# Kernel optimization log

Hardware: AMD Instinct MI355X
Metric: run time of the kernel (lower is better)

Reference implementation:

```python
import math
import jax, jax.numpy as jnp
import numpy as np

HEADS = 8
DIM_HEAD = 64
NUM_MEM_KV = 16


def alibi_slopes(heads):
    def pow2_slopes(n):
        start = 2 ** (-(2 ** -(math.log2(n) - 3)))
        return [start * (start ** i) for i in range(n)]
    if math.log2(heads).is_integer():
        return np.asarray(pow2_slopes(heads), dtype=np.float32)
    cp2 = 2 ** math.floor(math.log2(heads))
    extra = pow2_slopes(2 * cp2)[0::2][: heads - cp2]
    return np.asarray(pow2_slopes(cp2) + extra, dtype=np.float32)


def setup_inputs() -> dict:
    key = jax.random.key(0)
    ks = jax.random.split(key, 12)
    b, n, dim = 2, 2048, 512
    h, dh, mem = HEADS, DIM_HEAD, NUM_MEM_KV
    s = 0.02  # weight init scale for numerical sanity
    return {
        "x": jax.random.normal(ks[0], (b, n, dim), jnp.float32),
        "Wq": jax.random.normal(ks[1], (dim, h * dh), jnp.float32) * s,
        "Wk": jax.random.normal(ks[2], (dim, h * dh), jnp.float32) * s,
        "Wv": jax.random.normal(ks[3], (dim, h * dh), jnp.float32) * s,
        "mem_k": jax.random.normal(ks[4], (h, mem, dh), jnp.float32),
        "mem_v": jax.random.normal(ks[5], (h, mem, dh), jnp.float32),
        "pre_proj": jax.random.normal(ks[6], (h, h), jnp.float32),
        "post_proj": jax.random.normal(ks[7], (h, h), jnp.float32),
        "head_scale_params": jnp.ones((1, h, 1, 1), jnp.float32),
        "Wout": jax.random.normal(ks[8], (h * dh, dim), jnp.float32) * s,
        "bout": jnp.zeros((dim,), jnp.float32),
    }


def reference(x, Wq, Wk, Wv, mem_k, mem_v, pre_proj, post_proj,
              head_scale_params, Wout, bout):
    b, n, dim = x.shape
    h, dh, mem = HEADS, DIM_HEAD, NUM_MEM_KV
    scale = dh ** -0.5

    def split_heads(t):  # [b,n,h*dh] -> [b,h,n,dh]
        return t.reshape(b, n, h, dh).transpose(0, 2, 1, 3)

    q = split_heads(x @ Wq)
    k = split_heads(x @ Wk)
    v = split_heads(x @ Wv)

    # prepend learned memory key/values: k,v -> [b,h,mem+n,dh]
    k = jnp.concatenate([jnp.broadcast_to(mem_k, (b, h, mem, dh)), k], axis=2)
    v = jnp.concatenate([jnp.broadcast_to(mem_v, (b, h, mem, dh)), v], axis=2)
    j = mem + n

    dots = jnp.einsum('bhid,bhjd->bhij', q, k) * scale
    # talking heads (pre-softmax)
    dots = jnp.einsum('bhij,hk->bkij', dots, pre_proj)
    # alibi relative positional bias: arange(j) * slope per head
    slopes = jnp.asarray(alibi_slopes(h))  # [h]
    dots = dots + jnp.arange(j, dtype=dots.dtype)[None, None, None, :] * slopes[None, :, None, None]
    # causal mask (mem columns always visible); mask where col-mem > row
    neg = -jnp.finfo(dots.dtype).max
    causal = (jnp.arange(j)[None, :] - mem) > jnp.arange(n)[:, None]  # [n,j]
    dots = jnp.where(causal[None, None], neg, dots)

    attn = jax.nn.softmax(dots, axis=-1)
    # talking heads (post-softmax)
    attn = jnp.einsum('bhij,hk->bkij', attn, post_proj)

    out = jnp.einsum('bhij,bhjd->bhid', attn, v)
    out = out * head_scale_params
    out = out.transpose(0, 2, 1, 3).reshape(b, n, h * dh)
    return out @ Wout + bout
```

## Files before the change

### kernel.cpp

```cpp
#include <hip/hip_runtime.h>
#include <math.h>

namespace {
constexpr int B = 2;
constexpr int N = 2048;
constexpr int DIM = 512;
constexpr int H = 8;
constexpr int MEM = 16;
constexpr int J = MEM + N;
constexpr int CHUNK = 256;
constexpr int CMAX = 9;
constexpr float S2 = 0.125f * 1.4426950408889634f;
constexpr size_t EPB = 17170432;
}

typedef __attribute__((ext_vector_type(8))) short short8;
typedef __attribute__((ext_vector_type(4))) float floatx4;
typedef __attribute__((ext_vector_type(4))) unsigned short ushortx4;
typedef __attribute__((ext_vector_type(8))) unsigned short ushortx8;

__device__ inline unsigned short f2bf(float f) {
    unsigned int u = __float_as_uint(f);
    u += 0x7fffu + ((u >> 16) & 1u);
    return (unsigned short)(u >> 16);
}
__device__ inline unsigned int pk2bf(float a, float b) {
    return ((__float_as_uint(a) + 0x8000u) >> 16) |
           ((__float_as_uint(b) + 0x8000u) & 0xffff0000u);
}

__global__ __launch_bounds__(256)
void wt_conv(const float* __restrict__ Wq, const float* __restrict__ Wk,
             const float* __restrict__ Wv, const float* __restrict__ Wo,
             unsigned short* __restrict__ tq, unsigned short* __restrict__ tk,
             unsigned short* __restrict__ tv, unsigned short* __restrict__ to_)
{
    const int z = blockIdx.z;
    const float* __restrict__ W = (z == 0) ? Wq : (z == 1) ? Wk : (z == 2) ? Wv : Wo;
    unsigned short* __restrict__ WT = (z == 0) ? tq : (z == 1) ? tk : (z == 2) ? tv : to_;
    const int k0 = blockIdx.x * 64, n0 = blockIdx.y * 64;

    __shared__ __align__(16) unsigned short tile[64][72];
    const int t = threadIdx.x;
    const int rrow = t >> 4, rcol = (t & 15) * 4;
#pragma unroll
    for (int rr = 0; rr < 4; ++rr) {
        const int row = rrow + rr * 16;
        const float4 v = *(const float4*)(W + (size_t)(k0 + row) * DIM + n0 + rcol);
        tile[rcol + 0][row] = f2bf(v.x);
        tile[rcol + 1][row] = f2bf(v.y);
        tile[rcol + 2][row] = f2bf(v.z);
        tile[rcol + 3][row] = f2bf(v.w);
    }
    __syncthreads();
    const int orow = t >> 2, oseg = (t & 3) * 16;
    *(ushortx8*)(WT + (size_t)(n0 + orow) * DIM + k0 + oseg) =
        *(const ushortx8*)(&tile[orow][oseg]);
    *(ushortx8*)(WT + (size_t)(n0 + orow) * DIM + k0 + oseg + 8) =
        *(const ushortx8*)(&tile[orow][oseg + 8]);
}

__global__ __launch_bounds__(256)
void qkv_gemm(const float* __restrict__ x, const unsigned short* __restrict__ tq,
              const unsigned short* __restrict__ tk, const unsigned short* __restrict__ tv,
              unsigned short* __restrict__ q16, unsigned short* __restrict__ k16,
              unsigned short* __restrict__ vt16)
{
    const int which = blockIdx.z;
    const unsigned short* __restrict__ WT = (which == 0) ? tq : (which == 1) ? tk : tv;
    const int t = threadIdx.x;
    const int lane = t & 63, w = t >> 6;
    const int iL = lane & 15, quad = lane >> 4;
    const int mb = blockIdx.x * 64;
    const int n0 = blockIdx.y * 64;

    __shared__ __align__(16) unsigned short As[2][64][32];
    __shared__ __align__(16) unsigned short Bs[2][64][32];

    const int ar0 = t >> 3, as4 = (t & 7) * 4;
    const int br0 = t >> 2, bs8 = (t & 3) * 8;

    floatx4 acc[4];
#pragma unroll
    for (int ng = 0; ng < 4; ++ng) acc[ng] = (floatx4){0.f, 0.f, 0.f, 0.f};

    {
        const float4 v0 = *(const float4*)(x + (size_t)(mb + ar0) * DIM + as4);
        const float4 v1 = *(const float4*)(x + (size_t)(mb + ar0 + 32) * DIM + as4);
        ushortx4 o0 = { f2bf(v0.x), f2bf(v0.y), f2bf(v0.z), f2bf(v0.w) };
        ushortx4 o1 = { f2bf(v1.x), f2bf(v1.y), f2bf(v1.z), f2bf(v1.w) };
        *(ushortx4*)(&As[0][ar0][as4]) = o0;
        *(ushortx4*)(&As[0][ar0 + 32][as4]) = o1;
        *(ushortx8*)(&Bs[0][br0][bs8]) =
            *(const ushortx8*)(WT + (size_t)(n0 + br0) * DIM + bs8);
    }
    __syncthreads();

#pragma unroll
    for (int it = 0; it < 16; ++it) {
        const int buf = it & 1;
        if (it + 1 < 16) {
            const int k0 = (it + 1) * 32;
            const float4 v0 = *(const float4*)(x + (size_t)(mb + ar0) * DIM + k0 + as4);
            const float4 v1 = *(const float4*)(x + (size_t)(mb + ar0 + 32) * DIM + k0 + as4);
            const ushortx8 bv =
                *(const ushortx8*)(WT + (size_t)(n0 + br0) * DIM + k0 + bs8);
            ushortx4 o0 = { f2bf(v0.x), f2bf(v0.y), f2bf(v0.z), f2bf(v0.w) };
            ushortx4 o1 = { f2bf(v1.x), f2bf(v1.y), f2bf(v1.z), f2bf(v1.w) };
            *(ushortx4*)(&As[buf ^ 1][ar0][as4]) = o0;
            *(ushortx4*)(&As[buf ^ 1][ar0 + 32][as4]) = o1;
            *(ushortx8*)(&Bs[buf ^ 1][br0][bs8]) = bv;
        }
        const short8 af = *(const short8*)(&As[buf][w * 16 + iL][quad * 8]);
#pragma unroll
        for (int ng = 0; ng < 4; ++ng) {
            const short8 bf = *(const short8*)(&Bs[buf][ng * 16 + iL][quad * 8]);
            acc[ng] = __builtin_amdgcn_mfma_f32_16x16x32_bf16(af, bf, acc[ng], 0, 0, 0);
        }
        __syncthreads();
    }

    const int mbw = mb + w * 16;
    const int h0 = n0 >> 6;
    if (which == 2) {
#pragma unroll
        for (int ng = 0; ng < 4; ++ng) {
            const int d = ng * 16 + iL;
#pragma unroll
            for (int r = 0; r < 4; ++r) {
                const int m = mbw + quad * 4 + r;
                const int bb = m >> 11, ii = m & (N - 1);
                vt16[((size_t)(bb * H + h0) * 64 + d) * J + MEM + ii] = f2bf(acc[ng][r]);
            }
        }
    } else {
        unsigned short* dst = (which == 0) ? q16 : k16;
#pragma unroll
        for (int ng = 0; ng < 4; ++ng) {
            const int d = ng * 16 + iL;
#pragma unroll
            for (int r = 0; r < 4; ++r) {
                const int m = mbw + quad * 4 + r;
                const int bb = m >> 11, ii = m & (N - 1);
                const size_t rowbase = (which == 0)
                    ? ((size_t)(bb * H + h0) * N + ii)
                    : ((size_t)(bb * H + h0) * J + MEM + ii);
                dst[rowbase * 64 + d] = f2bf(acc[ng][r]);
            }
        }
    }
}

__global__ void memkv_copy(const float* __restrict__ mem_k, const float* __restrict__ mem_v,
                           unsigned short* __restrict__ k16, unsigned short* __restrict__ vt16)
{
    const int idx = blockIdx.x * 256 + threadIdx.x;
    if (idx >= H * MEM * 64) return;
    const int h0 = idx >> 10;
    const int rd = idx & 1023;
    const int r = rd >> 6, d = rd & 63;
    const unsigned short kk = f2bf(mem_k[idx]);
    const unsigned short vv = f2bf(mem_v[idx]);
#pragma unroll
    for (int bb = 0; bb < B; ++bb) {
        k16[((size_t)(bb * H + h0) * J + r) * 64 + d] = kk;
        vt16[((size_t)(bb * H + h0) * 64 + d) * J + r] = vv;
    }
}

__global__ __launch_bounds__(256)
void attn_scores(const unsigned short* __restrict__ qb, const unsigned short* __restrict__ kb,
                 const float* __restrict__ prep, float* __restrict__ lbuf,
                 unsigned short* __restrict__ e16)
{
    const int c = blockIdx.x, tt = 127 - blockIdx.y, b = blockIdx.z;
    const int i0 = tt * 16;
    const int jlim = i0 + 32;
    const int jstart = c * CHUNK;
    if (jstart >= jlim) return;
    const int jend = min(jstart + CHUNK, jlim);

    __shared__ __align__(16) unsigned short q_s[8][16][64];
    __shared__ __align__(16) float pre_s[64];
    const int t = threadIdx.x;
    if (t < 64) pre_s[t] = prep[t];
#pragma unroll
    for (int u4 = 0; u4 < 4; ++u4) {
        const int u = t + u4 * 256;
        const int h = u >> 7, rem = u & 127, i = rem >> 3, seg = (rem & 7) * 8;
        *(ushortx8*)(&q_s[h][i][seg]) =
            *(const ushortx8*)(qb + ((size_t)(b * H + h) * N + i0 + i) * 64 + seg);
    }
    __syncthreads();

    const int lane = t & 63, w = t >> 6;
    const int iL = lane & 15, quad = lane >> 4;
    const int i = i0 + iL;
    const size_t ebase = (size_t)b * EPB + (size_t)(8 * tt * tt + 24 * tt) * 128;

    float l_acc[8];
#pragma unroll
    for (int h1 = 0; h1 < 8; ++h1) l_acc[h1] = 0.f;

    bool any = false;
    for (int j0 = jstart + w * 16; j0 < jend; j0 += 64) {
        any = true;
        float dots[8][4];
#pragma unroll
        for (int h1 = 0; h1 < 8; ++h1)
#pragma unroll
            for (int r = 0; r < 4; ++r) dots[h1][r] = 0.f;

        const unsigned short* kp0 = kb + ((size_t)(b * H) * J + j0 + iL) * 64 + quad * 8;
        short8 kc0 = *(const short8*)kp0;
        short8 kc1 = *(const short8*)(kp0 + 32);
#pragma unroll
        for (int h0 = 0; h0 < 8; ++h0) {
            short8 kn0, kn1;
            if (h0 < 7) {
                const unsigned short* kpn =
                    kb + ((size_t)(b * H + h0 + 1) * J + j0 + iL) * 64 + quad * 8;
                kn0 = *(const short8*)kpn;
                kn1 = *(const short8*)(kpn + 32);
            }
            const short8 qf0 = *(const short8*)(&q_s[h0][iL][quad * 8]);
            const short8 qf1 = *(const short8*)(&q_s[h0][iL][quad * 8 + 32]);
            floatx4 a = {0.f, 0.f, 0.f, 0.f};
            a = __builtin_amdgcn_mfma_f32_16x16x32_bf16(kc0, qf0, a, 0, 0, 0);
            a = __builtin_amdgcn_mfma_f32_16x16x32_bf16(kc1, qf1, a, 0, 0, 0);
            const float4 pr0 = *(const float4*)(&pre_s[h0 * 8]);
            const float4 pr1 = *(const float4*)(&pre_s[h0 * 8 + 4]);
#pragma unroll
            for (int r = 0; r < 4; ++r) {
                const float av = a[r];
                dots[0][r] = fmaf(av, pr0.x, dots[0][r]);
                dots[1][r] = fmaf(av, pr0.y, dots[1][r]);
                dots[2][r] = fmaf(av, pr0.z, dots[2][r]);
                dots[3][r] = fmaf(av, pr0.w, dots[3][r]);
                dots[4][r] = fmaf(av, pr1.x, dots[4][r]);
                dots[5][r] = fmaf(av, pr1.y, dots[5][r]);
                dots[6][r] = fmaf(av, pr1.z, dots[6][r]);
                dots[7][r] = fmaf(av, pr1.w, dots[7][r]);
            }
            kc0 = kn0; kc1 = kn1;
        }

        unsigned int epk[4][4];
        float etmp[4];
#pragma unroll
        for (int h1 = 0; h1 < 8; ++h1) {
            const float slopeE = 1.4426950408889634f / (float)(2 << h1);
#pragma unroll
            for (int r = 0; r < 4; ++r) {
                const int j = j0 + quad * 4 + r;
                const bool vis = (j - MEM) <= i;
                const float e = vis ? exp2f(fmaf(dots[h1][r], S2, slopeE * (float)(j - i - MEM)))
                                    : 0.f;
                l_acc[h1] += e;
                if (h1 & 1) epk[r][h1 >> 1] = pk2bf(etmp[r], e);
                else        etmp[r] = e;
            }
        }
#pragma unroll
        for (int r = 0; r < 4; ++r) {
            uint4 o = make_uint4(epk[r][0], epk[r][1], epk[r][2], epk[r][3]);
            *(uint4*)(e16 + ebase + (size_t)((j0 + quad * 4 + r) * 16 + iL) * 8) = o;
        }
    }

#pragma unroll
    for (int h1 = 0; h1 < 8; ++h1) {
        float v = l_acc[h1];
        v += __shfl_xor(v, 16);
        v += __shfl_xor(v, 32);
        if (quad == 0 && any)
            atomicAdd(lbuf + ((size_t)(b * 128 + tt) * 8 + h1) * 16 + iL, v);
    }
}

__global__ __launch_bounds__(256)
void attn_pv2(const unsigned short* __restrict__ e16, const unsigned short* __restrict__ vt,
              const float* __restrict__ postp, const float* __restrict__ hsp,
              const float* __restrict__ lbuf, float* __restrict__ ao)
{
    const int c = blockIdx.x, tt = 127 - blockIdx.y, b = blockIdx.z;
    const int i0 = tt * 16;
    const int jlim = i0 + 32;
    const int jstart = c * CHUNK;
    if (jstart >= jlim) return;
    const int jend = min(jstart + CHUNK, jlim);
    const int nw = (jend - jstart + 31) >> 5;

    __shared__ __align__(16) unsigned short p2s[2][8][16][40];
    __shared__ __align__(16) float post_s[64];

    const int t = threadIdx.x;
    if (t < 64) post_s[t] = postp[t] * hsp[t & 7];

    const int lane = t & 63, w = t >> 6;
    const int iL = lane & 15, quad = lane >> 4;
    const int dW = w * 16 + iL;
    const int i_p = t & 15;
    const int jj = t >> 4;
    const size_t ebase = (size_t)b * EPB + (size_t)(8 * tt * tt + 24 * tt) * 128;

    float linv[8];
#pragma unroll
    for (int h1 = 0; h1 < 8; ++h1)
        linv[h1] = 1.0f / lbuf[((size_t)(b * 128 + tt) * 8 + h1) * 16 + i_p];

    floatx4 y[8];
#pragma unroll
    for (int h2 = 0; h2 < 8; ++h2) y[h2] = (floatx4){0.f, 0.f, 0.f, 0.f};

    ushortx8 evc[2], evn[2];
    {
        const int j0c = jstart + jj * 2;
        const int ja = min(j0c, jend - 1), jb2 = min(j0c + 1, jend - 1);
        evc[0] = *(const ushortx8*)(e16 + ebase + (size_t)(ja * 16 + i_p) * 8);
        evc[1] = *(const ushortx8*)(e16 + ebase + (size_t)(jb2 * 16 + i_p) * 8);
    }
    __syncthreads();

    for (int n = 0; n < nw; ++n) {
        const int jw0 = jstart + n * 32;
        {
            const int j0n = jstart + (n + 1) * 32 + jj * 2;
            const int ja = min(j0n, jend - 1), jb2 = min(j0n + 1, jend - 1);
            evn[0] = *(const ushortx8*)(e16 + ebase + (size_t)(ja * 16 + i_p) * 8);
            evn[1] = *(const ushortx8*)(e16 + ebase + (size_t)(jb2 * 16 + i_p) * 8);
        }
        float p2[2][8];
#pragma unroll
        for (int s = 0; s < 2; ++s) {
#pragma unroll
            for (int h2 = 0; h2 < 8; ++h2) p2[s][h2] = 0.f;
            const int j = jw0 + jj * 2 + s;
            if (j < jend) {
#pragma unroll
                for (int h1 = 0; h1 < 8; ++h1) {
                    const float e = __uint_as_float((unsigned int)(unsigned short)evc[s][h1] << 16)
                                    * linv[h1];
                    const float4 po0 = *(const float4*)(&post_s[h1 * 8]);
                    const float4 po1 = *(const float4*)(&post_s[h1 * 8 + 4]);
                    p2[s][0] = fmaf(e, po0.x, p2[s][0]);
                    p2[s][1] = fmaf(e, po0.y, p2[s][1]);
                    p2[s][2] = fmaf(e, po0.z, p2[s][2]);
                    p2[s][3] = fmaf(e, po0.w, p2[s][3]);
                    p2[s][4] = fmaf(e, po1.x, p2[s][4]);
                    p2[s][5] = fmaf(e, po1.y, p2[s][5]);
                    p2[s][6] = fmaf(e, po1.z, p2[s][6]);
                    p2[s][7] = fmaf(e, po1.w, p2[s][7]);
                }
            }
        }
        const int buf = n & 1;
#pragma unroll
        for (int h2 = 0; h2 < 8; ++h2)
            *(unsigned int*)(&p2s[buf][h2][i_p][jj * 2]) = pk2bf(p2[0][h2], p2[1][h2]);
        __syncthreads();

        int jbv = jw0 + quad * 8;
        if (jbv > J - 8) jbv = J - 8;
#pragma unroll
        for (int h2 = 0; h2 < 8; ++h2) {
            const short8 aF = *(const short8*)(&p2s[buf][h2][iL][quad * 8]);
            const short8 bF = *(const short8*)(vt + ((size_t)(b * H + h2) * 64 + dW) * J + jbv);
            y[h2] = __builtin_amdgcn_mfma_f32_16x16x32_bf16(aF, bF, y[h2], 0, 0, 0);
        }
        evc[0] = evn[0]; evc[1] = evn[1];
    }

#pragma unroll
    for (int h2 = 0; h2 < 8; ++h2) {
#pragma unroll
        for (int r = 0; r < 4; ++r) {
            const int ii = i0 + quad * 4 + r;
            atomicAdd(ao + ((size_t)b * N + ii) * DIM + h2 * 64 + dW, y[h2][r]);
        }
    }
}

__global__ __launch_bounds__(256)
void out_gemm(const float* __restrict__ ain, const unsigned short* __restrict__ WT,
              const float* __restrict__ bo, float* __restrict__ out)
{
    const int t = threadIdx.x;
    const int lane = t & 63, w = t >> 6;
    const int iL = lane & 15, quad = lane >> 4;
    const int mb = blockIdx.x * 64;
    const int n0 = blockIdx.y * 64;

    __shared__ __align__(16) unsigned short As[2][64][32];
    __shared__ __align__(16) unsigned short Bs[2][64][32];

    const int ar0 = t >> 3, as4 = (t & 7) * 4;
    const int br0 = t >> 2, bs8 = (t & 3) * 8;

    floatx4 acc[4];
#pragma unroll
    for (int ng = 0; ng < 4; ++ng) acc[ng] = (floatx4){0.f, 0.f, 0.f, 0.f};

    {
        const float4 v0 = *(const float4*)(ain + (size_t)(mb + ar0) * DIM + as4);
        const float4 v1 = *(const float4*)(ain + (size_t)(mb + ar0 + 32) * DIM + as4);
        ushortx4 o0 = { f2bf(v0.x), f2bf(v0.y), f2bf(v0.z), f2bf(v0.w) };
        ushortx4 o1 = { f2bf(v1.x), f2bf(v1.y), f2bf(v1.z), f2bf(v1.w) };
        *(ushortx4*)(&As[0][ar0][as4]) = o0;
        *(ushortx4*)(&As[0][ar0 + 32][as4]) = o1;
        *(ushortx8*)(&Bs[0][br0][bs8]) =
            *(const ushortx8*)(WT + (size_t)(n0 + br0) * DIM + bs8);
    }
    __syncthreads();

#pragma unroll
    for (int it = 0; it < 16; ++it) {
        const int buf = it & 1;
        if (it + 1 < 16) {
            const int k0 = (it + 1) * 32;
            const float4 v0 = *(const float4*)(ain + (size_t)(mb + ar0) * DIM + k0 + as4);
            const float4 v1 = *(const float4*)(ain + (size_t)(mb + ar0 + 32) * DIM + k0 + as4);
            const ushortx8 bv =
                *(const ushortx8*)(WT + (size_t)(n0 + br0) * DIM + k0 + bs8);
            ushortx4 o0 = { f2bf(v0.x), f2bf(v0.y), f2bf(v0.z), f2bf(v0.w) };
            ushortx4 o1 = { f2bf(v1.x), f2bf(v1.y), f2bf(v1.z), f2bf(v1.w) };
            *(ushortx4*)(&As[buf ^ 1][ar0][as4]) = o0;
            *(ushortx4*)(&As[buf ^ 1][ar0 + 32][as4]) = o1;
            *(ushortx8*)(&Bs[buf ^ 1][br0][bs8]) = bv;
        }
        const short8 af = *(const short8*)(&As[buf][w * 16 + iL][quad * 8]);
#pragma unroll
        for (int ng = 0; ng < 4; ++ng) {
            const short8 bf = *(const short8*)(&Bs[buf][ng * 16 + iL][quad * 8]);
            acc[ng] = __builtin_amdgcn_mfma_f32_16x16x32_bf16(af, bf, acc[ng], 0, 0, 0);
        }
        __syncthreads();
    }

    const int mbw = mb + w * 16;
#pragma unroll
    for (int ng = 0; ng < 4; ++ng) {
        const int n = n0 + ng * 16 + iL;
        const float bias = bo[n];
#pragma unroll
        for (int r = 0; r < 4; ++r) {
            const int m = mbw + quad * 4 + r;
            out[(size_t)m * DIM + n] = acc[ng][r] + bias;
        }
    }
}

extern "C" void kernel_launch(void* const* d_in, const int* in_sizes, int n_in,
                              void* d_out, int out_size, void* d_ws, size_t ws_size,
                              hipStream_t stream)
{
    (void)in_sizes; (void)n_in; (void)out_size; (void)ws_size;
    const float* x      = (const float*)d_in[0];
    const float* Wq     = (const float*)d_in[1];
    const float* Wk     = (const float*)d_in[2];
    const float* Wv     = (const float*)d_in[3];
    const float* mem_k  = (const float*)d_in[4];
    const float* mem_v  = (const float*)d_in[5];
    const float* pre_p  = (const float*)d_in[6];
    const float* post_p = (const float*)d_in[7];
    const float* hs     = (const float*)d_in[8];
    const float* Wo     = (const float*)d_in[9];
    const float* bo     = (const float*)d_in[10];
    float* out = (float*)d_out;

    constexpr size_t NAO  = (size_t)B * N * DIM;
    constexpr size_t NLB  = (size_t)B * 128 * H * 16;
    constexpr size_t NW   = (size_t)DIM * DIM;
    constexpr size_t NQ   = (size_t)B * H * N * 64;
    constexpr size_t NK   = (size_t)B * H * J * 64;

    float* ws = (float*)d_ws;
    float* ao   = ws;
    float* lbuf = ao + NAO;
    unsigned short* wtq  = (unsigned short*)(lbuf + NLB);
    unsigned short* wtk  = wtq + NW;
    unsigned short* wtv  = wtk + NW;
    unsigned short* wto  = wtv + NW;
    unsigned short* q16  = wto + NW;
    unsigned short* k16  = q16 + NQ;
    unsigned short* v16  = k16 + NK;
    unsigned short* e16  = v16 + NK;

    wt_conv<<<dim3(8, 8, 4), 256, 0, stream>>>(Wq, Wk, Wv, Wo, wtq, wtk, wtv, wto);
    qkv_gemm<<<dim3(64, 8, 3), 256, 0, stream>>>(x, wtq, wtk, wtv, q16, k16, v16);
    memkv_copy<<<dim3(32), 256, 0, stream>>>(mem_k, mem_v, k16, v16);
    hipMemsetAsync(ao, 0, (NAO + NLB) * sizeof(float), stream);
    attn_scores<<<dim3(CMAX, 128, B), 256, 0, stream>>>(q16, k16, pre_p, lbuf, e16);
    attn_pv2<<<dim3(CMAX, 128, B), 256, 0, stream>>>(e16, v16, post_p, hs, lbuf, ao);
    out_gemm<<<dim3(64, 8), 256, 0, stream>>>(ao, wto, bo, out);
}
```

Measured before the change: 236.8 us.

## Replace j-chunk split with one block per row tile, dropping atomics and memset

The attention score and PV kernels no longer split the key dimension into 256-wide chunks across a 3D grid. Each kernel now runs one block per (batch, 16-row tile) with an interleaved block order, and walks the full causal range itself. This removes the atomicAdd reductions, replacing them with an LDS reduction and plain stores, and drops the memset. The PV kernel processes 64-wide windows, double-buffers e loads, and prefetches V fragments. The K prefetch depth in the score kernel goes from one head ahead to two. The cost is only 256 blocks with long, uneven per-block work, which lowers parallelism and leaves load balance dependent on the block ordering.

```diff
diff --git a/kernel.cpp b/kernel.cpp
--- a/kernel.cpp
+++ b/kernel.cpp
@@ -8,8 +8,6 @@
 constexpr int H = 8;
 constexpr int MEM = 16;
 constexpr int J = MEM + N;
-constexpr int CHUNK = 256;
-constexpr int CMAX = 9;
 constexpr float S2 = 0.125f * 1.4426950408889634f;
 constexpr size_t EPB = 17170432;
 }
@@ -27,6 +25,12 @@
 __device__ inline unsigned int pk2bf(float a, float b) {
     return ((__float_as_uint(a) + 0x8000u) >> 16) |
            ((__float_as_uint(b) + 0x8000u) & 0xffff0000u);
+}
+
+__device__ inline void decode_bt(int id, int& b, int& tt) {
+    b = (id >> 2) & 1;
+    const int ttidx = ((id >> 3) << 2) | (id & 3);
+    tt = 127 - ttidx;
 }
 
 __global__ __launch_bounds__(256)
@@ -168,20 +172,19 @@
     }
 }
 
-__global__ __launch_bounds__(256)
+__global__ __launch_bounds__(256, 1)
 void attn_scores(const unsigned short* __restrict__ qb, const unsigned short* __restrict__ kb,
                  const float* __restrict__ prep, float* __restrict__ lbuf,
                  unsigned short* __restrict__ e16)
 {
-    const int c = blockIdx.x, tt = 127 - blockIdx.y, b = blockIdx.z;
+    int b, tt;
+    decode_bt(blockIdx.x, b, tt);
     const int i0 = tt * 16;
-    const int jlim = i0 + 32;
-    const int jstart = c * CHUNK;
-    if (jstart >= jlim) return;
-    const int jend = min(jstart + CHUNK, jlim);
+    const int jend = i0 + 32;
 
     __shared__ __align__(16) unsigned short q_s[8][16][64];
-    __shared__ __align__(16) float pre_s[64];
+    __shared__ float pre_s[64];
+    __shared__ float lred[4][8][16];
     const int t = threadIdx.x;
     if (t < 64) pre_s[t] = prep[t];
 #pragma unroll
@@ -202,32 +205,32 @@
 #pragma unroll
     for (int h1 = 0; h1 < 8; ++h1) l_acc[h1] = 0.f;
 
-    bool any = false;
-    for (int j0 = jstart + w * 16; j0 < jend; j0 += 64) {
-        any = true;
+    for (int j0 = w * 16; j0 < jend; j0 += 64) {
         float dots[8][4];
 #pragma unroll
         for (int h1 = 0; h1 < 8; ++h1)
 #pragma unroll
             for (int r = 0; r < 4; ++r) dots[h1][r] = 0.f;
 
-        const unsigned short* kp0 = kb + ((size_t)(b * H) * J + j0 + iL) * 64 + quad * 8;
-        short8 kc0 = *(const short8*)kp0;
-        short8 kc1 = *(const short8*)(kp0 + 32);
+        const unsigned short* kbase = kb + ((size_t)(b * H) * J + j0 + iL) * 64 + quad * 8;
+        const size_t hstride = (size_t)J * 64;
+        short8 ka0 = *(const short8*)(kbase);
+        short8 ka1 = *(const short8*)(kbase + 32);
+        short8 kb0_ = *(const short8*)(kbase + hstride);
+        short8 kb1_ = *(const short8*)(kbase + hstride + 32);
 #pragma unroll
         for (int h0 = 0; h0 < 8; ++h0) {
-            short8 kn0, kn1;
-            if (h0 < 7) {
-                const unsigned short* kpn =
-                    kb + ((size_t)(b * H + h0 + 1) * J + j0 + iL) * 64 + quad * 8;
-                kn0 = *(const short8*)kpn;
-                kn1 = *(const short8*)(kpn + 32);
+            short8 kc0_, kc1_;
+            if (h0 < 6) {
+                const unsigned short* kpn = kbase + (size_t)(h0 + 2) * hstride;
+                kc0_ = *(const short8*)(kpn);
+                kc1_ = *(const short8*)(kpn + 32);
             }
             const short8 qf0 = *(const short8*)(&q_s[h0][iL][quad * 8]);
             const short8 qf1 = *(const short8*)(&q_s[h0][iL][quad * 8 + 32]);
             floatx4 a = {0.f, 0.f, 0.f, 0.f};
-            a = __builtin_amdgcn_mfma_f32_16x16x32_bf16(kc0, qf0, a, 0, 0, 0);
-            a = __builtin_amdgcn_mfma_f32_16x16x32_bf16(kc1, qf1, a, 0, 0, 0);
+            a = __builtin_amdgcn_mfma_f32_16x16x32_bf16(ka0, qf0, a, 0, 0, 0);
+            a = __builtin_amdgcn_mfma_f32_16x16x32_bf16(ka1, qf1, a, 0, 0, 0);
             const float4 pr0 = *(const float4*)(&pre_s[h0 * 8]);
             const float4 pr1 = *(const float4*)(&pre_s[h0 * 8 + 4]);
 #pragma unroll
@@ -242,7 +245,7 @@
                 dots[6][r] = fmaf(av, pr1.z, dots[6][r]);
                 dots[7][r] = fmaf(av, pr1.w, dots[7][r]);
             }
-            kc0 = kn0; kc1 = kn1;
+            ka0 = kb0_; ka1 = kb1_; kb0_ = kc0_; kb1_ = kc1_;
         }
 
         unsigned int epk[4][4];
@@ -273,26 +276,29 @@
         float v = l_acc[h1];
         v += __shfl_xor(v, 16);
         v += __shfl_xor(v, 32);
-        if (quad == 0 && any)
-            atomicAdd(lbuf + ((size_t)(b * 128 + tt) * 8 + h1) * 16 + iL, v);
-    }
-}
-
-__global__ __launch_bounds__(256)
+        if (quad == 0) lred[w][h1][iL] = v;
+    }
+    __syncthreads();
+    if (t < 128) {
+        const int h1 = t >> 4, i2 = t & 15;
+        lbuf[((size_t)(b * 128 + tt) * 8 + h1) * 16 + i2] =
+            lred[0][h1][i2] + lred[1][h1][i2] + lred[2][h1][i2] + lred[3][h1][i2];
+    }
+}
+
+__global__ __launch_bounds__(256, 1)
 void attn_pv2(const unsigned short* __restrict__ e16, const unsigned short* __restrict__ vt,
               const float* __restrict__ postp, const float* __restrict__ hsp,
               const float* __restrict__ lbuf, float* __restrict__ ao)
 {
-    const int c = blockIdx.x, tt = 127 - blockIdx.y, b = blockIdx.z;
+    int b, tt;
+    decode_bt(blockIdx.x, b, tt);
     const int i0 = tt * 16;
-    const int jlim = i0 + 32;
-    const int jstart = c * CHUNK;
-    if (jstart >= jlim) return;
-    const int jend = min(jstart + CHUNK, jlim);
-    const int nw = (jend - jstart + 31) >> 5;
-
-    __shared__ __align__(16) unsigned short p2s[2][8][16][40];
-    __shared__ __align__(16) float post_s[64];
+    const int jend = i0 + 32;
+    const int nw = (jend + 63) >> 6;
+
+    __shared__ __align__(16) unsigned short p2s[2][8][16][72];
+    __shared__ float post_s[64];
 
     const int t = threadIdx.x;
     if (t < 64) post_s[t] = postp[t] * hsp[t & 7];
@@ -303,6 +309,7 @@
     const int i_p = t & 15;
     const int jj = t >> 4;
     const size_t ebase = (size_t)b * EPB + (size_t)(8 * tt * tt + 24 * tt) * 128;
+    const unsigned short* __restrict__ ep = e16 + ebase + (size_t)i_p * 8;
 
     float linv[8];
 #pragma unroll
@@ -313,34 +320,47 @@
 #pragma unroll
     for (int h2 = 0; h2 < 8; ++h2) y[h2] = (floatx4){0.f, 0.f, 0.f, 0.f};
 
-    ushortx8 evc[2], evn[2];
+    ushortx8 ev0[4], ev1[4];
     {
-        const int j0c = jstart + jj * 2;
-        const int ja = min(j0c, jend - 1), jb2 = min(j0c + 1, jend - 1);
-        evc[0] = *(const ushortx8*)(e16 + ebase + (size_t)(ja * 16 + i_p) * 8);
-        evc[1] = *(const ushortx8*)(e16 + ebase + (size_t)(jb2 * 16 + i_p) * 8);
+        const int j00 = jj * 4;
+#pragma unroll
+        for (int s = 0; s < 4; ++s) {
+            const int j = min(j00 + s, jend - 1);
+            ev0[s] = *(const ushortx8*)(ep + (size_t)j * 128);
+        }
+        if (nw > 1) {
+            const int j01 = 64 + jj * 4;
+#pragma unroll
+            for (int s = 0; s < 4; ++s) {
+                const int j = min(j01 + s, jend - 1);
+                ev1[s] = *(const ushortx8*)(ep + (size_t)j * 128);
+            }
+        }
     }
     __syncthreads();
 
-    for (int n = 0; n < nw; ++n) {
-        const int jw0 = jstart + n * 32;
-        {
-            const int j0n = jstart + (n + 1) * 32 + jj * 2;
-            const int ja = min(j0n, jend - 1), jb2 = min(j0n + 1, jend - 1);
-            evn[0] = *(const ushortx8*)(e16 + ebase + (size_t)(ja * 16 + i_p) * 8);
-            evn[1] = *(const ushortx8*)(e16 + ebase + (size_t)(jb2 * 16 + i_p) * 8);
-        }
-        float p2[2][8];
-#pragma unroll
-        for (int s = 0; s < 2; ++s) {
+    auto window = [&](const int n, ushortx8 (&ev)[4], const int buf) {
+        const int jw0 = n * 64;
+        short8 bF0[8], bF1[8];
+        int jb0 = jw0 + quad * 8;      if (jb0 > J - 8) jb0 = J - 8;
+        int jb1 = jw0 + 32 + quad * 8; if (jb1 > J - 8) jb1 = J - 8;
+#pragma unroll
+        for (int h2 = 0; h2 < 8; ++h2) {
+            const unsigned short* vp = vt + ((size_t)(b * H + h2) * 64 + dW) * J;
+            bF0[h2] = *(const short8*)(vp + jb0);
+            bF1[h2] = *(const short8*)(vp + jb1);
+        }
+        float p2[4][8];
+#pragma unroll
+        for (int s = 0; s < 4; ++s) {
 #pragma unroll
             for (int h2 = 0; h2 < 8; ++h2) p2[s][h2] = 0.f;
-            const int j = jw0 + jj * 2 + s;
+            const int j = jw0 + jj * 4 + s;
             if (j < jend) {
 #pragma unroll
                 for (int h1 = 0; h1 < 8; ++h1) {
-                    const float e = __uint_as_float((unsigned int)(unsigned short)evc[s][h1] << 16)
-                                    * linv[h1];
+                    const float e = __uint_as_float(
+                        (unsigned int)(unsigned short)ev[s][h1] << 16) * linv[h1];
                     const float4 po0 = *(const float4*)(&post_s[h1 * 8]);
                     const float4 po1 = *(const float4*)(&post_s[h1 * 8 + 4]);
                     p2[s][0] = fmaf(e, po0.x, p2[s][0]);
@@ -354,31 +374,47 @@
                 }
             }
         }
-        const int buf = n & 1;
-#pragma unroll
-        for (int h2 = 0; h2 < 8; ++h2)
-            *(unsigned int*)(&p2s[buf][h2][i_p][jj * 2]) = pk2bf(p2[0][h2], p2[1][h2]);
+        if (n + 2 < nw) {
+            const int j0n = (n + 2) * 64 + jj * 4;
+#pragma unroll
+            for (int s = 0; s < 4; ++s) {
+                const int j = min(j0n + s, jend - 1);
+                ev[s] = *(const ushortx8*)(ep + (size_t)j * 128);
+            }
+        }
+#pragma unroll
+        for (int h2 = 0; h2 < 8; ++h2) {
+            uint2 o;
+            o.x = pk2bf(p2[0][h2], p2[1][h2]);
+            o.y = pk2bf(p2[2][h2], p2[3][h2]);
+            *(uint2*)(&p2s[buf][h2][i_p][jj * 4]) = o;
+        }
         __syncthreads();
-
-        int jbv = jw0 + quad * 8;
-        if (jbv > J - 8) jbv = J - 8;
 #pragma unroll
         for (int h2 = 0; h2 < 8; ++h2) {
-            const short8 aF = *(const short8*)(&p2s[buf][h2][iL][quad * 8]);
-            const short8 bF = *(const short8*)(vt + ((size_t)(b * H + h2) * 64 + dW) * J + jbv);
-            y[h2] = __builtin_amdgcn_mfma_f32_16x16x32_bf16(aF, bF, y[h2], 0, 0, 0);
-        }
-        evc[0] = evn[0]; evc[1] = evn[1];
-    }
-
-#pragma unroll
-    for (int h2 = 0; h2 < 8; ++h2) {
+            const short8 aF0 = *(const short8*)(&p2s[buf][h2][iL][quad * 8]);
+            const short8 aF1 = *(const short8*)(&p2s[buf][h2][iL][32 + quad * 8]);
+            y[h2] = __builtin_amdgcn_mfma_f32_16x16x32_bf16(aF0, bF0[h2], y[h2], 0, 0, 0);
+            y[h2] = __builtin_amdgcn_mfma_f32_16x16x32_bf16(aF1, bF1[h2], y[h2], 0, 0, 0);
+        }
+    };
+
+    int n = 0;
+    for (;;) {
+        window(n, ev0, 0);
+        if (n + 1 >= nw) break;
+        window(n + 1, ev1, 1);
+        n += 2;
+        if (n >= nw) break;
+    }
+
+#pragma unroll
+    for (int h2 = 0; h2 < 8; ++h2)
 #pragma unroll
         for (int r = 0; r < 4; ++r) {
             const int ii = i0 + quad * 4 + r;
-            atomicAdd(ao + ((size_t)b * N + ii) * DIM + h2 * 64 + dW, y[h2][r]);
-        }
-    }
+            ao[((size_t)b * N + ii) * DIM + h2 * 64 + dW] = y[h2][r];
+        }
 }
 
 __global__ __launch_bounds__(256)
@@ -489,8 +525,7 @@
     wt_conv<<<dim3(8, 8, 4), 256, 0, stream>>>(Wq, Wk, Wv, Wo, wtq, wtk, wtv, wto);
     qkv_gemm<<<dim3(64, 8, 3), 256, 0, stream>>>(x, wtq, wtk, wtv, q16, k16, v16);
     memkv_copy<<<dim3(32), 256, 0, stream>>>(mem_k, mem_v, k16, v16);
-    hipMemsetAsync(ao, 0, (NAO + NLB) * sizeof(float), stream);
-    attn_scores<<<dim3(CMAX, 128, B), 256, 0, stream>>>(q16, k16, pre_p, lbuf, e16);
-    attn_pv2<<<dim3(CMAX, 128, B), 256, 0, stream>>>(e16, v16, post_p, hs, lbuf, ao);
+    attn_scores<<<dim3(256), 256, 0, stream>>>(q16, k16, pre_p, lbuf, e16);
+    attn_pv2<<<dim3(256), 256, 0, stream>>>(e16, v16, post_p, hs, lbuf, ao);
     out_gemm<<<dim3(64, 8), 256, 0, stream>>>(ao, wto, bo, out);
 }
```

Result: slower. 322.7 us (+36.3%).

## Recompute scores in PV kernel instead of materializing exp scores buffer

Applied to the files above, without the earlier changes.

The score kernel becomes a normalizer-only pass that no longer writes the bf16 exp-score tensor. A new fused kernel recomputes QK^T, the talking-heads mixes, alibi bias and exp, then normalizes, applies the post-mix and runs the PV MFMA directly from shared memory. This trades the large global write and read of the intermediate scores for computing QK^T and exp twice. The K prefetch is deepened to two heads ahead, and the grid order is changed so the row-tile index varies fastest.

```diff
diff --git a/kernel.cpp b/kernel.cpp
--- a/kernel.cpp
+++ b/kernel.cpp
@@ -11,7 +11,6 @@
 constexpr int CHUNK = 256;
 constexpr int CMAX = 9;
 constexpr float S2 = 0.125f * 1.4426950408889634f;
-constexpr size_t EPB = 17170432;
 }
 
 typedef __attribute__((ext_vector_type(8))) short short8;
@@ -169,19 +168,18 @@
 }
 
 __global__ __launch_bounds__(256)
-void attn_scores(const unsigned short* __restrict__ qb, const unsigned short* __restrict__ kb,
-                 const float* __restrict__ prep, float* __restrict__ lbuf,
-                 unsigned short* __restrict__ e16)
-{
-    const int c = blockIdx.x, tt = 127 - blockIdx.y, b = blockIdx.z;
+void attn_lpass(const unsigned short* __restrict__ qb, const unsigned short* __restrict__ kb,
+                const float* __restrict__ prep, float* __restrict__ lbuf)
+{
+    const int tt = blockIdx.x, c = blockIdx.y, b = blockIdx.z;
     const int i0 = tt * 16;
     const int jlim = i0 + 32;
     const int jstart = c * CHUNK;
     if (jstart >= jlim) return;
-    const int jend = min(jstart + CHUNK, jlim);
+    const int jend_c = min(jstart + CHUNK, jlim);
 
     __shared__ __align__(16) unsigned short q_s[8][16][64];
-    __shared__ __align__(16) float pre_s[64];
+    __shared__ float pre_s[64];
     const int t = threadIdx.x;
     if (t < 64) pre_s[t] = prep[t];
 #pragma unroll
@@ -196,14 +194,13 @@
     const int lane = t & 63, w = t >> 6;
     const int iL = lane & 15, quad = lane >> 4;
     const int i = i0 + iL;
-    const size_t ebase = (size_t)b * EPB + (size_t)(8 * tt * tt + 24 * tt) * 128;
 
     float l_acc[8];
 #pragma unroll
     for (int h1 = 0; h1 < 8; ++h1) l_acc[h1] = 0.f;
 
     bool any = false;
-    for (int j0 = jstart + w * 16; j0 < jend; j0 += 64) {
+    for (int j0 = jstart + w * 16; j0 < jend_c; j0 += 64) {
         any = true;
         float dots[8][4];
 #pragma unroll
@@ -211,23 +208,25 @@
 #pragma unroll
             for (int r = 0; r < 4; ++r) dots[h1][r] = 0.f;
 
-        const unsigned short* kp0 = kb + ((size_t)(b * H) * J + j0 + iL) * 64 + quad * 8;
-        short8 kc0 = *(const short8*)kp0;
-        short8 kc1 = *(const short8*)(kp0 + 32);
+        const unsigned short* kbase = kb + ((size_t)(b * H) * J + j0 + iL) * 64 + quad * 8;
+        const size_t hstride = (size_t)J * 64;
+        short8 ka0 = *(const short8*)(kbase);
+        short8 ka1 = *(const short8*)(kbase + 32);
+        short8 kb0_ = *(const short8*)(kbase + hstride);
+        short8 kb1_ = *(const short8*)(kbase + hstride + 32);
 #pragma unroll
         for (int h0 = 0; h0 < 8; ++h0) {
-            short8 kn0, kn1;
-            if (h0 < 7) {
-                const unsigned short* kpn =
-                    kb + ((size_t)(b * H + h0 + 1) * J + j0 + iL) * 64 + quad * 8;
-                kn0 = *(const short8*)kpn;
-                kn1 = *(const short8*)(kpn + 32);
+            short8 kc0_, kc1_;
+            if (h0 < 6) {
+                const unsigned short* kpn = kbase + (size_t)(h0 + 2) * hstride;
+                kc0_ = *(const short8*)(kpn);
+                kc1_ = *(const short8*)(kpn + 32);
             }
             const short8 qf0 = *(const short8*)(&q_s[h0][iL][quad * 8]);
             const short8 qf1 = *(const short8*)(&q_s[h0][iL][quad * 8 + 32]);
             floatx4 a = {0.f, 0.f, 0.f, 0.f};
-            a = __builtin_amdgcn_mfma_f32_16x16x32_bf16(kc0, qf0, a, 0, 0, 0);
-            a = __builtin_amdgcn_mfma_f32_16x16x32_bf16(kc1, qf1, a, 0, 0, 0);
+            a = __builtin_amdgcn_mfma_f32_16x16x32_bf16(ka0, qf0, a, 0, 0, 0);
+            a = __builtin_amdgcn_mfma_f32_16x16x32_bf16(ka1, qf1, a, 0, 0, 0);
             const float4 pr0 = *(const float4*)(&pre_s[h0 * 8]);
             const float4 pr1 = *(const float4*)(&pre_s[h0 * 8 + 4]);
 #pragma unroll
@@ -242,11 +241,9 @@
                 dots[6][r] = fmaf(av, pr1.z, dots[6][r]);
                 dots[7][r] = fmaf(av, pr1.w, dots[7][r]);
             }
-            kc0 = kn0; kc1 = kn1;
-        }
-
-        unsigned int epk[4][4];
-        float etmp[4];
+            ka0 = kb0_; ka1 = kb1_; kb0_ = kc0_; kb1_ = kc1_;
+        }
+
 #pragma unroll
         for (int h1 = 0; h1 < 8; ++h1) {
             const float slopeE = 1.4426950408889634f / (float)(2 << h1);
@@ -257,14 +254,7 @@
                 const float e = vis ? exp2f(fmaf(dots[h1][r], S2, slopeE * (float)(j - i - MEM)))
                                     : 0.f;
                 l_acc[h1] += e;
-                if (h1 & 1) epk[r][h1 >> 1] = pk2bf(etmp[r], e);
-                else        etmp[r] = e;
-            }
-        }
-#pragma unroll
-        for (int r = 0; r < 4; ++r) {
-            uint4 o = make_uint4(epk[r][0], epk[r][1], epk[r][2], epk[r][3]);
-            *(uint4*)(e16 + ebase + (size_t)((j0 + quad * 4 + r) * 16 + iL) * 8) = o;
+            }
         }
     }
 
@@ -279,106 +269,164 @@
 }
 
 __global__ __launch_bounds__(256)
-void attn_pv2(const unsigned short* __restrict__ e16, const unsigned short* __restrict__ vt,
-              const float* __restrict__ postp, const float* __restrict__ hsp,
-              const float* __restrict__ lbuf, float* __restrict__ ao)
-{
-    const int c = blockIdx.x, tt = 127 - blockIdx.y, b = blockIdx.z;
+void attn_fused(const unsigned short* __restrict__ qb, const unsigned short* __restrict__ kb,
+                const unsigned short* __restrict__ vt, const float* __restrict__ prep,
+                const float* __restrict__ postp, const float* __restrict__ hsp,
+                const float* __restrict__ lbuf, float* __restrict__ ao)
+{
+    const int tt = blockIdx.x, c = blockIdx.y, b = blockIdx.z;
     const int i0 = tt * 16;
     const int jlim = i0 + 32;
     const int jstart = c * CHUNK;
     if (jstart >= jlim) return;
-    const int jend = min(jstart + CHUNK, jlim);
-    const int nw = (jend - jstart + 31) >> 5;
-
-    __shared__ __align__(16) unsigned short p2s[2][8][16][40];
-    __shared__ __align__(16) float post_s[64];
+    const int jend_c = min(jstart + CHUNK, jlim);
+    const int nwc = (jend_c - jstart + 63) >> 6;
+
+    __shared__ __align__(16) unsigned short q_s[8][16][64];
+    __shared__ __align__(16) unsigned short p_s[2][8][16][72];
+    __shared__ float pre_s[64];
+    __shared__ float post_s[64];
 
     const int t = threadIdx.x;
-    if (t < 64) post_s[t] = postp[t] * hsp[t & 7];
+    if (t < 64) {
+        pre_s[t]  = prep[t];
+        post_s[t] = postp[t] * hsp[t & 7];
+    }
+#pragma unroll
+    for (int u4 = 0; u4 < 4; ++u4) {
+        const int u = t + u4 * 256;
+        const int h = u >> 7, rem = u & 127, i = rem >> 3, seg = (rem & 7) * 8;
+        *(ushortx8*)(&q_s[h][i][seg]) =
+            *(const ushortx8*)(qb + ((size_t)(b * H + h) * N + i0 + i) * 64 + seg);
+    }
 
     const int lane = t & 63, w = t >> 6;
     const int iL = lane & 15, quad = lane >> 4;
+    const int i = i0 + iL;
     const int dW = w * 16 + iL;
-    const int i_p = t & 15;
-    const int jj = t >> 4;
-    const size_t ebase = (size_t)b * EPB + (size_t)(8 * tt * tt + 24 * tt) * 128;
 
     float linv[8];
 #pragma unroll
     for (int h1 = 0; h1 < 8; ++h1)
-        linv[h1] = 1.0f / lbuf[((size_t)(b * 128 + tt) * 8 + h1) * 16 + i_p];
+        linv[h1] = 1.0f / lbuf[((size_t)(b * 128 + tt) * 8 + h1) * 16 + iL];
 
     floatx4 y[8];
 #pragma unroll
     for (int h2 = 0; h2 < 8; ++h2) y[h2] = (floatx4){0.f, 0.f, 0.f, 0.f};
 
-    ushortx8 evc[2], evn[2];
-    {
-        const int j0c = jstart + jj * 2;
-        const int ja = min(j0c, jend - 1), jb2 = min(j0c + 1, jend - 1);
-        evc[0] = *(const ushortx8*)(e16 + ebase + (size_t)(ja * 16 + i_p) * 8);
-        evc[1] = *(const ushortx8*)(e16 + ebase + (size_t)(jb2 * 16 + i_p) * 8);
-    }
     __syncthreads();
 
-    for (int n = 0; n < nw; ++n) {
-        const int jw0 = jstart + n * 32;
-        {
-            const int j0n = jstart + (n + 1) * 32 + jj * 2;
-            const int ja = min(j0n, jend - 1), jb2 = min(j0n + 1, jend - 1);
-            evn[0] = *(const ushortx8*)(e16 + ebase + (size_t)(ja * 16 + i_p) * 8);
-            evn[1] = *(const ushortx8*)(e16 + ebase + (size_t)(jb2 * 16 + i_p) * 8);
-        }
-        float p2[2][8];
-#pragma unroll
-        for (int s = 0; s < 2; ++s) {
-#pragma unroll
-            for (int h2 = 0; h2 < 8; ++h2) p2[s][h2] = 0.f;
-            const int j = jw0 + jj * 2 + s;
-            if (j < jend) {
-#pragma unroll
-                for (int h1 = 0; h1 < 8; ++h1) {
-                    const float e = __uint_as_float((unsigned int)(unsigned short)evc[s][h1] << 16)
-                                    * linv[h1];
-                    const float4 po0 = *(const float4*)(&post_s[h1 * 8]);
-                    const float4 po1 = *(const float4*)(&post_s[h1 * 8 + 4]);
-                    p2[s][0] = fmaf(e, po0.x, p2[s][0]);
-                    p2[s][1] = fmaf(e, po0.y, p2[s][1]);
-                    p2[s][2] = fmaf(e, po0.z, p2[s][2]);
-                    p2[s][3] = fmaf(e, po0.w, p2[s][3]);
-                    p2[s][4] = fmaf(e, po1.x, p2[s][4]);
-                    p2[s][5] = fmaf(e, po1.y, p2[s][5]);
-                    p2[s][6] = fmaf(e, po1.z, p2[s][6]);
-                    p2[s][7] = fmaf(e, po1.w, p2[s][7]);
-                }
-            }
-        }
+    const size_t hstride = (size_t)J * 64;
+
+    for (int n = 0; n < nwc; ++n) {
+        const int jw0 = jstart + n * 64;
         const int buf = n & 1;
+
+        int jb0 = jw0 + quad * 8;      if (jb0 > J - 8) jb0 = J - 8;
+        int jb1 = jw0 + 32 + quad * 8; if (jb1 > J - 8) jb1 = J - 8;
+        short8 bF0[8], bF1[8];
+#pragma unroll
+        for (int h2 = 0; h2 < 8; ++h2) {
+            const unsigned short* vp = vt + ((size_t)(b * H + h2) * 64 + dW) * J;
+            bF0[h2] = *(const short8*)(vp + jb0);
+            bF1[h2] = *(const short8*)(vp + jb1);
+        }
+
+        const int j0 = jw0 + w * 16;
+        const int jr = min(j0 + iL, J - 1);
+        float dots[8][4];
+#pragma unroll
+        for (int h1 = 0; h1 < 8; ++h1)
+#pragma unroll
+            for (int r = 0; r < 4; ++r) dots[h1][r] = 0.f;
+
+        const unsigned short* kbase = kb + ((size_t)(b * H) * J + jr) * 64 + quad * 8;
+        short8 ka0 = *(const short8*)(kbase);
+        short8 ka1 = *(const short8*)(kbase + 32);
+        short8 kb0_ = *(const short8*)(kbase + hstride);
+        short8 kb1_ = *(const short8*)(kbase + hstride + 32);
+#pragma unroll
+        for (int h0 = 0; h0 < 8; ++h0) {
+            short8 kc0_, kc1_;
+            if (h0 < 6) {
+                const unsigned short* kpn = kbase + (size_t)(h0 + 2) * hstride;
+                kc0_ = *(const short8*)(kpn);
+                kc1_ = *(const short8*)(kpn + 32);
+            }
+            const short8 qf0 = *(const short8*)(&q_s[h0][iL][quad * 8]);
+            const short8 qf1 = *(const short8*)(&q_s[h0][iL][quad * 8 + 32]);
+            floatx4 a = {0.f, 0.f, 0.f, 0.f};
+            a = __builtin_amdgcn_mfma_f32_16x16x32_bf16(ka0, qf0, a, 0, 0, 0);
+            a = __builtin_amdgcn_mfma_f32_16x16x32_bf16(ka1, qf1, a, 0, 0, 0);
+            const float4 pr0 = *(const float4*)(&pre_s[h0 * 8]);
+            const float4 pr1 = *(const float4*)(&pre_s[h0 * 8 + 4]);
+#pragma unroll
+            for (int r = 0; r < 4; ++r) {
+                const float av = a[r];
+                dots[0][r] = fmaf(av, pr0.x, dots[0][r]);
+                dots[1][r] = fmaf(av, pr0.y, dots[1][r]);
+                dots[2][r] = fmaf(av, pr0.z, dots[2][r]);
+                dots[3][r] = fmaf(av, pr0.w, dots[3][r]);
+                dots[4][r] = fmaf(av, pr1.x, dots[4][r]);
+                dots[5][r] = fmaf(av, pr1.y, dots[5][r]);
+                dots[6][r] = fmaf(av, pr1.z, dots[6][r]);
+                dots[7][r] = fmaf(av, pr1.w, dots[7][r]);
+            }
+            ka0 = kb0_; ka1 = kb1_; kb0_ = kc0_; kb1_ = kc1_;
+        }
+
+        float p2[8][4];
 #pragma unroll
         for (int h2 = 0; h2 < 8; ++h2)
-            *(unsigned int*)(&p2s[buf][h2][i_p][jj * 2]) = pk2bf(p2[0][h2], p2[1][h2]);
+#pragma unroll
+            for (int r = 0; r < 4; ++r) p2[h2][r] = 0.f;
+#pragma unroll
+        for (int h1 = 0; h1 < 8; ++h1) {
+            const float slopeE = 1.4426950408889634f / (float)(2 << h1);
+            const float4 po0 = *(const float4*)(&post_s[h1 * 8]);
+            const float4 po1 = *(const float4*)(&post_s[h1 * 8 + 4]);
+#pragma unroll
+            for (int r = 0; r < 4; ++r) {
+                const int j = j0 + quad * 4 + r;
+                const bool vis = (j - MEM) <= i;
+                const float e = vis ? exp2f(fmaf(dots[h1][r], S2, slopeE * (float)(j - i - MEM)))
+                                    : 0.f;
+                const float en = e * linv[h1];
+                p2[0][r] = fmaf(en, po0.x, p2[0][r]);
+                p2[1][r] = fmaf(en, po0.y, p2[1][r]);
+                p2[2][r] = fmaf(en, po0.z, p2[2][r]);
+                p2[3][r] = fmaf(en, po0.w, p2[3][r]);
+                p2[4][r] = fmaf(en, po1.x, p2[4][r]);
+                p2[5][r] = fmaf(en, po1.y, p2[5][r]);
+                p2[6][r] = fmaf(en, po1.z, p2[6][r]);
+                p2[7][r] = fmaf(en, po1.w, p2[7][r]);
+            }
+        }
+#pragma unroll
+        for (int h2 = 0; h2 < 8; ++h2) {
+            uint2 o;
+            o.x = pk2bf(p2[h2][0], p2[h2][1]);
+            o.y = pk2bf(p2[h2][2], p2[h2][3]);
+            *(uint2*)(&p_s[buf][h2][iL][w * 16 + quad * 4]) = o;
+        }
         __syncthreads();
 
-        int jbv = jw0 + quad * 8;
-        if (jbv > J - 8) jbv = J - 8;
 #pragma unroll
         for (int h2 = 0; h2 < 8; ++h2) {
-            const short8 aF = *(const short8*)(&p2s[buf][h2][iL][quad * 8]);
-            const short8 bF = *(const short8*)(vt + ((size_t)(b * H + h2) * 64 + dW) * J + jbv);
-            y[h2] = __builtin_amdgcn_mfma_f32_16x16x32_bf16(aF, bF, y[h2], 0, 0, 0);
-        }
-        evc[0] = evn[0]; evc[1] = evn[1];
-    }
-
-#pragma unroll
-    for (int h2 = 0; h2 < 8; ++h2) {
+            const short8 aF0 = *(const short8*)(&p_s[buf][h2][iL][quad * 8]);
+            const short8 aF1 = *(const short8*)(&p_s[buf][h2][iL][32 + quad * 8]);
+            y[h2] = __builtin_amdgcn_mfma_f32_16x16x32_bf16(aF0, bF0[h2], y[h2], 0, 0, 0);
+            y[h2] = __builtin_amdgcn_mfma_f32_16x16x32_bf16(aF1, bF1[h2], y[h2], 0, 0, 0);
+        }
+    }
+
+#pragma unroll
+    for (int h2 = 0; h2 < 8; ++h2)
 #pragma unroll
         for (int r = 0; r < 4; ++r) {
             const int ii = i0 + quad * 4 + r;
             atomicAdd(ao + ((size_t)b * N + ii) * DIM + h2 * 64 + dW, y[h2][r]);
         }
-    }
 }
 
 __global__ __launch_bounds__(256)
@@ -484,13 +532,13 @@
     unsigned short* q16  = wto + NW;
     unsigned short* k16  = q16 + NQ;
     unsigned short* v16  = k16 + NK;
-    unsigned short* e16  = v16 + NK;
 
     wt_conv<<<dim3(8, 8, 4), 256, 0, stream>>>(Wq, Wk, Wv, Wo, wtq, wtk, wtv, wto);
     qkv_gemm<<<dim3(64, 8, 3), 256, 0, stream>>>(x, wtq, wtk, wtv, q16, k16, v16);
     memkv_copy<<<dim3(32), 256, 0, stream>>>(mem_k, mem_v, k16, v16);
     hipMemsetAsync(ao, 0, (NAO + NLB) * sizeof(float), stream);
-    attn_scores<<<dim3(CMAX, 128, B), 256, 0, stream>>>(q16, k16, pre_p, lbuf, e16);
-    attn_pv2<<<dim3(CMAX, 128, B), 256, 0, stream>>>(e16, v16, post_p, hs, lbuf, ao);
+    attn_lpass<<<dim3(128, CMAX, B), 256, 0, stream>>>(q16, k16, pre_p, lbuf);
+    attn_fused<<<dim3(128, CMAX, B), 256, 0, stream>>>(q16, k16, v16, pre_p, post_p, hs,
+                                                       lbuf, ao);
     out_gemm<<<dim3(64, 8), 256, 0, stream>>>(ao, wto, bo, out);
 }
```

New measurement: 313.9 us. 32.5% more time.
